# Optimization experiments

Measured on AMD Instinct MI355X. Metric: run time of the kernel, lower is better.

The kernel has to match this reference:

```python
import jax, jax.numpy as jnp
import numpy as np

B, S, D, H, O = 64, 512, 1024, 1024, 1024

def setup_inputs() -> dict:
    key = jax.random.key(0)
    k1, k2, k3 = jax.random.split(key, 3)
    x = jax.random.normal(k1, (B, S, D), dtype=jnp.float32)
    Wg = jax.random.normal(k2, (D + H, 3 * H), dtype=jnp.float32) / np.sqrt(D + H)
    bg = jnp.zeros((3 * H,), dtype=jnp.float32)
    Wc = jax.random.normal(k3, (H, O), dtype=jnp.float32) / np.sqrt(H)
    bc = jnp.zeros((O,), dtype=jnp.float32)
    return {"x": x, "Wg": Wg, "bg": bg, "Wc": Wc, "bc": bc}

def reference(x, Wg, bg, Wc, bc):
    # GRU cell matching the torch module: network = Linear(D+H, 3H)
    def step(h, x_t):
        combined = jnp.concatenate([x_t, h], axis=1)            # [B, D+H]
        gates = combined @ Wg + bg                              # [B, 3H]
        r_g, z_g, n_g = jnp.split(gates, 3, axis=1)
        r = jax.nn.sigmoid(r_g)
        z = jax.nn.sigmoid(z_g)
        n = jnp.tanh(n_g + r * h)
        h_next = (1 - z) * n + z * h
        return h_next, h_next

    h0 = jnp.zeros((x.shape[0], Wc.shape[0]), dtype=x.dtype)
    xs = jnp.swapaxes(x, 0, 1)                                  # [S, B, D]
    _, hs = jax.lax.scan(step, h0, xs)                          # hs: [S, B, H]
    outputs = jnp.swapaxes(hs, 0, 1)                            # [B, S, H]
    return outputs @ Wc + bc                                    # [B, S, O]
```

## Files before the change

kernel.cpp:

```cpp
#include <hip/hip_runtime.h>
#include <hip/hip_bf16.h>
#include <stdint.h>

#define BB   64
#define SS   512
#define DD   1024
#define HH   1024
#define TH3  3072
#define TCH  32

using frag8 = __attribute__((ext_vector_type(8))) short;
using f32x4 = __attribute__((ext_vector_type(4))) float;

__device__ __forceinline__ void split_bf16(float v, short& hi, short& lo) {
    uint32_t u = __float_as_uint(v);
    uint32_t uh = u & 0xFFFF0000u;
    float fl = v - __uint_as_float(uh);
    hi = (short)(uh >> 16);
    lo = (short)(__float_as_uint(fl) >> 16);
}

__device__ __forceinline__ float bf2f(unsigned short u) {
    union { uint32_t i; float f; } v;
    v.i = ((uint32_t)u) << 16;
    return v.f;
}

__global__ __launch_bounds__(256) void prep_w(
    const float* __restrict__ Wg, short* __restrict__ Wt_hi,
    short* __restrict__ Wt_lo)
{
    int idx = blockIdx.x * 256 + threadIdx.x;
    int lane = idx & 63;
    int f = idx >> 6;
    int kt = f & 63;
    int fg = f >> 6;
    int g = fg % 3;
    int jb = fg / 3;
    int krow = kt * 32 + (lane >> 4) * 8;
    int col = g * HH + jb * 16 + (lane & 15);
    size_t dst = (size_t)f * 512 + (size_t)lane * 8;
#pragma unroll
    for (int j = 0; j < 8; ++j) {
        float v = Wg[(size_t)(krow + j) * TH3 + col];
        short hi, lo;
        split_bf16(v, hi, lo);
        Wt_hi[dst + j] = hi;
        Wt_lo[dst + j] = lo;
    }
}

__global__ __launch_bounds__(256) void gx_gemm(
    const short* __restrict__ Wt_hi, const short* __restrict__ Wt_lo,
    const float* __restrict__ x,
    const float* __restrict__ bg,
    float* __restrict__ gx,
    int t0)
{
    const int tid = threadIdx.x;
    const int lane = tid & 63;
    const int w = tid >> 6;
    const int jb = blockIdx.x & 63;
    const int tl = blockIdx.x >> 6;
    const int t = t0 + tl;
    const int m0 = w * 16;
    const int mrow = m0 + (lane & 15);
    const int kq = (lane >> 4) * 8;

    f32x4 accr = {0.f, 0.f, 0.f, 0.f};
    f32x4 accz = {0.f, 0.f, 0.f, 0.f};
    f32x4 accn = {0.f, 0.f, 0.f, 0.f};
    const size_t fbase = (size_t)jb * 3 * 64;
    const float* xrow = x + ((size_t)mrow * SS + t) * DD;

    for (int kt = 0; kt < 32; ++kt) {
        const float* xp = xrow + kt * 32 + kq;
        float xv[8];
        *(float4*)&xv[0] = *(const float4*)xp;
        *(float4*)&xv[4] = *(const float4*)(xp + 4);
        frag8 a_hi, a_lo;
#pragma unroll
        for (int j = 0; j < 8; ++j) {
            short hi, lo;
            split_bf16(xv[j], hi, lo);
            a_hi[j] = hi;
            a_lo[j] = lo;
        }
#pragma unroll
        for (int g = 0; g < 3; ++g) {
            size_t base = (fbase + (size_t)g * 64 + kt) * 512 + (size_t)lane * 8;
            frag8 b_hi = *(const frag8*)(Wt_hi + base);
            frag8 b_lo = *(const frag8*)(Wt_lo + base);
            f32x4 acc = (g == 0) ? accr : (g == 1) ? accz : accn;
            acc = __builtin_amdgcn_mfma_f32_16x16x32_bf16(a_hi, b_hi, acc, 0, 0, 0);
            acc = __builtin_amdgcn_mfma_f32_16x16x32_bf16(a_hi, b_lo, acc, 0, 0, 0);
            acc = __builtin_amdgcn_mfma_f32_16x16x32_bf16(a_lo, b_hi, acc, 0, 0, 0);
            if (g == 0) accr = acc; else if (g == 1) accz = acc; else accn = acc;
        }
    }

    const int col = jb * 16 + (lane & 15);
    const int rbase = m0 + (lane >> 4) * 4;
    const float b_r = bg[col];
    const float b_z = bg[HH + col];
    const float b_n = bg[2 * HH + col];
#pragma unroll
    for (int reg = 0; reg < 4; ++reg) {
        int m = rbase + reg;
        float* gp = gx + ((size_t)tl * BB + m) * TH3;
        gp[col] = accr[reg] + b_r;
        gp[HH + col] = accz[reg] + b_z;
        gp[2 * HH + col] = accn[reg] + b_n;
    }
}

__global__ __launch_bounds__(256) void gru_step_h(
    const short* __restrict__ Wt_hi, const short* __restrict__ Wt_lo,
    const float* __restrict__ gx,
    const float* __restrict__ h_f,
    const short* __restrict__ h_hi,
    const short* __restrict__ h_lo,
    float* __restrict__ hn_f,
    short* __restrict__ hn_hi, short* __restrict__ hn_lo,
    __hip_bfloat16* __restrict__ hs,
    int t, int tl)
{
    __shared__ float red[12][256];

    const int tid = threadIdx.x;
    const int lane = tid & 63;
    const int w = tid >> 6;
    const int jb = blockIdx.x & 63;
    const int mt = blockIdx.x >> 6;
    const int m0 = mt * 16;
    const int mrow = m0 + (lane & 15);
    const int kq = (lane >> 4) * 8;

    const int lv = tid >> 2;
    const int reg = tid & 3;
    const int ecol = jb * 16 + (lv & 15);
    const int em = m0 + ((lv >> 4) << 2) + reg;
    const float* gp = gx + ((size_t)tl * BB + em) * TH3 + ecol;
    const float gxr = gp[0];
    const float gxz = gp[HH];
    const float gxn = gp[2 * HH];
    const float hold = h_f[(size_t)em * HH + ecol];

    f32x4 accr = {0.f, 0.f, 0.f, 0.f};
    f32x4 accz = {0.f, 0.f, 0.f, 0.f};
    f32x4 accn = {0.f, 0.f, 0.f, 0.f};
    const size_t fbase = (size_t)jb * 3 * 64;
    const short* hrh = h_hi + (size_t)mrow * HH;
    const short* hrl = h_lo + (size_t)mrow * HH;

#pragma unroll
    for (int i = 0; i < 8; ++i) {
        const int kt = w * 8 + i;
        frag8 a_hi = *(const frag8*)(hrh + kt * 32 + kq);
        frag8 a_lo = *(const frag8*)(hrl + kt * 32 + kq);
#pragma unroll
        for (int g = 0; g < 3; ++g) {
            size_t base = (fbase + (size_t)g * 64 + 32 + kt) * 512 + (size_t)lane * 8;
            frag8 b_hi = *(const frag8*)(Wt_hi + base);
            frag8 b_lo = *(const frag8*)(Wt_lo + base);
            f32x4 acc = (g == 0) ? accr : (g == 1) ? accz : accn;
            acc = __builtin_amdgcn_mfma_f32_16x16x32_bf16(a_hi, b_hi, acc, 0, 0, 0);
            acc = __builtin_amdgcn_mfma_f32_16x16x32_bf16(a_hi, b_lo, acc, 0, 0, 0);
            acc = __builtin_amdgcn_mfma_f32_16x16x32_bf16(a_lo, b_hi, acc, 0, 0, 0);
            if (g == 0) accr = acc; else if (g == 1) accz = acc; else accn = acc;
        }
    }

    *(f32x4*)&red[w * 3 + 0][lane * 4] = accr;
    *(f32x4*)&red[w * 3 + 1][lane * 4] = accz;
    *(f32x4*)&red[w * 3 + 2][lane * 4] = accn;
    __syncthreads();

    float rg = gxr + red[0][tid] + red[3][tid] + red[6][tid] + red[9][tid];
    float zg = gxz + red[1][tid] + red[4][tid] + red[7][tid] + red[10][tid];
    float ng = gxn + red[2][tid] + red[5][tid] + red[8][tid] + red[11][tid];

    float r = 1.f / (1.f + __expf(-rg));
    float z = 1.f / (1.f + __expf(-zg));
    float na = ng + r * hold;
    float n = 1.f - 2.f / (1.f + __expf(2.f * na));
    float hn = (1.f - z) * n + z * hold;

    hn_f[(size_t)em * HH + ecol] = hn;
    short hi, lo;
    split_bf16(hn, hi, lo);
    hn_hi[(size_t)em * HH + ecol] = hi;
    hn_lo[(size_t)em * HH + ecol] = lo;
    hs[((size_t)em * SS + t) * HH + ecol] = __float2bfloat16(hn);
}

#define BM 128
#define BN 128
#define BK 8

__global__ __launch_bounds__(256) void out_gemm(
    const __hip_bfloat16* __restrict__ A, const float* __restrict__ Bm,
    const float* __restrict__ bias, float* __restrict__ C)
{
    __shared__ float As[BK][BM + 4];
    __shared__ float Bs[BK][BN + 4];

    const int tid = threadIdx.x;
    const int bx = blockIdx.x;
    const int by = blockIdx.y;

    const int arow = tid >> 1;
    const int acol = (tid & 1) * 4;
    const int brow = tid >> 5;
    const int bcol = (tid & 31) * 4;

    const int tx8 = (tid & 15) * 8;
    const int ty8 = (tid >> 4) * 8;

    float acc[8][8];
#pragma unroll
    for (int i = 0; i < 8; ++i)
#pragma unroll
        for (int j = 0; j < 8; ++j) acc[i][j] = 0.f;

    const unsigned short* Aptr =
        (const unsigned short*)A + (size_t)(by * BM + arow) * HH + acol;
    const float* Bptr = Bm + (size_t)brow * HH + bx * BN + bcol;

    for (int k0 = 0; k0 < HH; k0 += BK) {
        ushort4 au = *(const ushort4*)Aptr;
        float4 bv = *(const float4*)Bptr;
        As[acol + 0][arow] = bf2f(au.x);
        As[acol + 1][arow] = bf2f(au.y);
        As[acol + 2][arow] = bf2f(au.z);
        As[acol + 3][arow] = bf2f(au.w);
        *(float4*)&Bs[brow][bcol] = bv;
        __syncthreads();

#pragma unroll
        for (int k = 0; k < BK; ++k) {
            float a[8], bvv[8];
            *(float4*)&a[0] = *(const float4*)&As[k][ty8];
            *(float4*)&a[4] = *(const float4*)&As[k][ty8 + 4];
            *(float4*)&bvv[0] = *(const float4*)&Bs[k][tx8];
            *(float4*)&bvv[4] = *(const float4*)&Bs[k][tx8 + 4];
#pragma unroll
            for (int i = 0; i < 8; ++i)
#pragma unroll
                for (int j = 0; j < 8; ++j)
                    acc[i][j] += a[i] * bvv[j];
        }
        __syncthreads();
        Aptr += BK;
        Bptr += (size_t)BK * HH;
    }

    float bv8[8];
#pragma unroll
    for (int j = 0; j < 8; ++j) bv8[j] = bias[bx * BN + tx8 + j];

#pragma unroll
    for (int i = 0; i < 8; ++i) {
        float* cptr = C + (size_t)(by * BM + ty8 + i) * HH + bx * BN + tx8;
        float4 v0, v1;
        v0.x = acc[i][0] + bv8[0];
        v0.y = acc[i][1] + bv8[1];
        v0.z = acc[i][2] + bv8[2];
        v0.w = acc[i][3] + bv8[3];
        v1.x = acc[i][4] + bv8[4];
        v1.y = acc[i][5] + bv8[5];
        v1.z = acc[i][6] + bv8[6];
        v1.w = acc[i][7] + bv8[7];
        *(float4*)cptr = v0;
        *(float4*)(cptr + 4) = v1;
    }
}

extern "C" void kernel_launch(void* const* d_in, const int* in_sizes, int n_in,
                              void* d_out, int out_size, void* d_ws, size_t ws_size,
                              hipStream_t stream) {
    const float* x  = (const float*)d_in[0];
    const float* Wg = (const float*)d_in[1];
    const float* bg = (const float*)d_in[2];
    const float* Wc = (const float*)d_in[3];
    const float* bc = (const float*)d_in[4];
    float* out = (float*)d_out;

    char* ws = (char*)d_ws;
    __hip_bfloat16* hs = (__hip_bfloat16*)ws;
    short* Wt_hi = (short*)(ws + 67108864);
    short* Wt_lo = (short*)(ws + 67108864 + 12582912);
    char* state = ws + 67108864 + 2 * 12582912;
    const size_t SET = 524288;
    float* gx = (float*)(state + 2 * SET);

    float* hf[2];  short* hhi[2]; short* hlo[2];
    for (int p = 0; p < 2; ++p) {
        hf[p]  = (float*)(state + p * SET);
        hhi[p] = (short*)(state + p * SET + 262144);
        hlo[p] = (short*)(state + p * SET + 393216);
    }

    hipMemsetAsync(state, 0, SET, stream);

    prep_w<<<3072, 256, 0, stream>>>(Wg, Wt_hi, Wt_lo);

    for (int t0 = 0; t0 < SS; t0 += TCH) {
        gx_gemm<<<TCH * 64, 256, 0, stream>>>(Wt_hi, Wt_lo, x, bg, gx, t0);
        for (int tl = 0; tl < TCH; ++tl) {
            int t = t0 + tl;
            int c = t & 1, n = c ^ 1;
            gru_step_h<<<256, 256, 0, stream>>>(
                Wt_hi, Wt_lo, gx,
                hf[c], hhi[c], hlo[c],
                hf[n], hhi[n], hlo[n],
                hs, t, tl);
        }
    }

    {
        dim3 g2(HH / BN, (BB * SS) / BM);
        out_gemm<<<g2, 256, 0, stream>>>(hs, Wc, bc, out);
    }
}
```

Measured before the change: 6.752 ms.

## Move output projection to bf16 MFMA and register-tile the input-gate GEMM

The scalar FP32 shared-memory output GEMM is replaced by an MFMA kernel. It uses bf16 hs and a hi/lo split of Wc (two MFMAs per tile), with Wc pre-swizzled into fragment layout by a new prep kernel that reuses the gx workspace. The gx_gemm kernel is also register-tiled so that each wave computes 2x2 16x16 tiles, which reuses A and B fragments and launches fewer blocks. Dropping the lo term for hs keeps the earlier bf16 rounding of hs while taking the output GEMM off the vector ALUs, but it adds another split-precision approximation for Wc.

```diff
diff --git a/kernel.cpp b/kernel.cpp
--- a/kernel.cpp
+++ b/kernel.cpp
@@ -18,12 +18,6 @@
     float fl = v - __uint_as_float(uh);
     hi = (short)(uh >> 16);
     lo = (short)(__float_as_uint(fl) >> 16);
-}
-
-__device__ __forceinline__ float bf2f(unsigned short u) {
-    union { uint32_t i; float f; } v;
-    v.i = ((uint32_t)u) << 16;
-    return v.f;
 }
 
 __global__ __launch_bounds__(256) void prep_w(
@@ -50,6 +44,28 @@
     }
 }
 
+__global__ __launch_bounds__(256) void prep_wc(
+    const float* __restrict__ Wc, short* __restrict__ Wct_hi,
+    short* __restrict__ Wct_lo)
+{
+    int idx = blockIdx.x * 256 + threadIdx.x;
+    int lane = idx & 63;
+    int f = idx >> 6;
+    int kt = f & 31;
+    int jb = f >> 5;
+    int krow = kt * 32 + (lane >> 4) * 8;
+    int col = jb * 16 + (lane & 15);
+    size_t dst = (size_t)f * 512 + (size_t)lane * 8;
+#pragma unroll
+    for (int j = 0; j < 8; ++j) {
+        float v = Wc[(size_t)(krow + j) * HH + col];
+        short hi, lo;
+        split_bf16(v, hi, lo);
+        Wct_hi[dst + j] = hi;
+        Wct_lo[dst + j] = lo;
+    }
+}
+
 __global__ __launch_bounds__(256) void gx_gemm(
     const short* __restrict__ Wt_hi, const short* __restrict__ Wt_lo,
     const float* __restrict__ x,
@@ -60,57 +76,79 @@
     const int tid = threadIdx.x;
     const int lane = tid & 63;
     const int w = tid >> 6;
-    const int jb = blockIdx.x & 63;
-    const int tl = blockIdx.x >> 6;
+    const int jbg = blockIdx.x & 15;
+    const int tl = blockIdx.x >> 4;
     const int t = t0 + tl;
-    const int m0 = w * 16;
-    const int mrow = m0 + (lane & 15);
+    const int m0 = (w & 1) * 32;
+    const int jbb = jbg * 4 + (w >> 1) * 2;
     const int kq = (lane >> 4) * 8;
 
-    f32x4 accr = {0.f, 0.f, 0.f, 0.f};
-    f32x4 accz = {0.f, 0.f, 0.f, 0.f};
-    f32x4 accn = {0.f, 0.f, 0.f, 0.f};
-    const size_t fbase = (size_t)jb * 3 * 64;
-    const float* xrow = x + ((size_t)mrow * SS + t) * DD;
+    f32x4 acc[2][2][3];
+#pragma unroll
+    for (int mi = 0; mi < 2; ++mi)
+#pragma unroll
+        for (int jp = 0; jp < 2; ++jp)
+#pragma unroll
+            for (int g = 0; g < 3; ++g)
+                acc[mi][jp][g] = (f32x4){0.f, 0.f, 0.f, 0.f};
+
+    const float* xr0 = x + ((size_t)(m0 + (lane & 15)) * SS + t) * DD;
+    const float* xr1 = xr0 + (size_t)16 * SS * DD;
 
     for (int kt = 0; kt < 32; ++kt) {
-        const float* xp = xrow + kt * 32 + kq;
-        float xv[8];
-        *(float4*)&xv[0] = *(const float4*)xp;
-        *(float4*)&xv[4] = *(const float4*)(xp + 4);
-        frag8 a_hi, a_lo;
-#pragma unroll
-        for (int j = 0; j < 8; ++j) {
-            short hi, lo;
-            split_bf16(xv[j], hi, lo);
-            a_hi[j] = hi;
-            a_lo[j] = lo;
-        }
+        frag8 ah[2], al[2];
+#pragma unroll
+        for (int mi = 0; mi < 2; ++mi) {
+            const float* xp = (mi == 0 ? xr0 : xr1) + kt * 32 + kq;
+            float xv[8];
+            *(float4*)&xv[0] = *(const float4*)xp;
+            *(float4*)&xv[4] = *(const float4*)(xp + 4);
+#pragma unroll
+            for (int j = 0; j < 8; ++j) {
+                short hi, lo;
+                split_bf16(xv[j], hi, lo);
+                ah[mi][j] = hi;
+                al[mi][j] = lo;
+            }
+        }
+#pragma unroll
+        for (int jp = 0; jp < 2; ++jp) {
+#pragma unroll
+            for (int g = 0; g < 3; ++g) {
+                size_t base =
+                    (((size_t)(jbb + jp) * 3 + g) * 64 + kt) * 512 + (size_t)lane * 8;
+                frag8 bh = *(const frag8*)(Wt_hi + base);
+                frag8 bl = *(const frag8*)(Wt_lo + base);
+#pragma unroll
+                for (int mi = 0; mi < 2; ++mi) {
+                    f32x4 a = acc[mi][jp][g];
+                    a = __builtin_amdgcn_mfma_f32_16x16x32_bf16(ah[mi], bh, a, 0, 0, 0);
+                    a = __builtin_amdgcn_mfma_f32_16x16x32_bf16(ah[mi], bl, a, 0, 0, 0);
+                    a = __builtin_amdgcn_mfma_f32_16x16x32_bf16(al[mi], bh, a, 0, 0, 0);
+                    acc[mi][jp][g] = a;
+                }
+            }
+        }
+    }
+
+    const int lcol = lane & 15;
+    const int rq = (lane >> 4) * 4;
+#pragma unroll
+    for (int jp = 0; jp < 2; ++jp) {
+        const int col = (jbb + jp) * 16 + lcol;
 #pragma unroll
         for (int g = 0; g < 3; ++g) {
-            size_t base = (fbase + (size_t)g * 64 + kt) * 512 + (size_t)lane * 8;
-            frag8 b_hi = *(const frag8*)(Wt_hi + base);
-            frag8 b_lo = *(const frag8*)(Wt_lo + base);
-            f32x4 acc = (g == 0) ? accr : (g == 1) ? accz : accn;
-            acc = __builtin_amdgcn_mfma_f32_16x16x32_bf16(a_hi, b_hi, acc, 0, 0, 0);
-            acc = __builtin_amdgcn_mfma_f32_16x16x32_bf16(a_hi, b_lo, acc, 0, 0, 0);
-            acc = __builtin_amdgcn_mfma_f32_16x16x32_bf16(a_lo, b_hi, acc, 0, 0, 0);
-            if (g == 0) accr = acc; else if (g == 1) accz = acc; else accn = acc;
-        }
-    }
-
-    const int col = jb * 16 + (lane & 15);
-    const int rbase = m0 + (lane >> 4) * 4;
-    const float b_r = bg[col];
-    const float b_z = bg[HH + col];
-    const float b_n = bg[2 * HH + col];
-#pragma unroll
-    for (int reg = 0; reg < 4; ++reg) {
-        int m = rbase + reg;
-        float* gp = gx + ((size_t)tl * BB + m) * TH3;
-        gp[col] = accr[reg] + b_r;
-        gp[HH + col] = accz[reg] + b_z;
-        gp[2 * HH + col] = accn[reg] + b_n;
+            const float bias = bg[g * HH + col];
+#pragma unroll
+            for (int mi = 0; mi < 2; ++mi) {
+#pragma unroll
+                for (int reg = 0; reg < 4; ++reg) {
+                    int m = m0 + mi * 16 + rq + reg;
+                    gx[((size_t)tl * BB + m) * TH3 + g * HH + col] =
+                        acc[mi][jp][g][reg] + bias;
+                }
+            }
+        }
     }
 }
 
@@ -194,85 +232,64 @@
     hs[((size_t)em * SS + t) * HH + ecol] = __float2bfloat16(hn);
 }
 
-#define BM 128
-#define BN 128
-#define BK 8
-
-__global__ __launch_bounds__(256) void out_gemm(
-    const __hip_bfloat16* __restrict__ A, const float* __restrict__ Bm,
-    const float* __restrict__ bias, float* __restrict__ C)
-{
-    __shared__ float As[BK][BM + 4];
-    __shared__ float Bs[BK][BN + 4];
-
+__global__ __launch_bounds__(256) void out_mfma(
+    const short* __restrict__ Wct_hi, const short* __restrict__ Wct_lo,
+    const __hip_bfloat16* __restrict__ hs,
+    const float* __restrict__ bc, float* __restrict__ out)
+{
     const int tid = threadIdx.x;
-    const int bx = blockIdx.x;
-    const int by = blockIdx.y;
-
-    const int arow = tid >> 1;
-    const int acol = (tid & 1) * 4;
-    const int brow = tid >> 5;
-    const int bcol = (tid & 31) * 4;
-
-    const int tx8 = (tid & 15) * 8;
-    const int ty8 = (tid >> 4) * 8;
-
-    float acc[8][8];
-#pragma unroll
-    for (int i = 0; i < 8; ++i)
-#pragma unroll
-        for (int j = 0; j < 8; ++j) acc[i][j] = 0.f;
-
-    const unsigned short* Aptr =
-        (const unsigned short*)A + (size_t)(by * BM + arow) * HH + acol;
-    const float* Bptr = Bm + (size_t)brow * HH + bx * BN + bcol;
-
-    for (int k0 = 0; k0 < HH; k0 += BK) {
-        ushort4 au = *(const ushort4*)Aptr;
-        float4 bv = *(const float4*)Bptr;
-        As[acol + 0][arow] = bf2f(au.x);
-        As[acol + 1][arow] = bf2f(au.y);
-        As[acol + 2][arow] = bf2f(au.z);
-        As[acol + 3][arow] = bf2f(au.w);
-        *(float4*)&Bs[brow][bcol] = bv;
-        __syncthreads();
-
-#pragma unroll
-        for (int k = 0; k < BK; ++k) {
-            float a[8], bvv[8];
-            *(float4*)&a[0] = *(const float4*)&As[k][ty8];
-            *(float4*)&a[4] = *(const float4*)&As[k][ty8 + 4];
-            *(float4*)&bvv[0] = *(const float4*)&Bs[k][tx8];
-            *(float4*)&bvv[4] = *(const float4*)&Bs[k][tx8 + 4];
-#pragma unroll
-            for (int i = 0; i < 8; ++i)
-#pragma unroll
-                for (int j = 0; j < 8; ++j)
-                    acc[i][j] += a[i] * bvv[j];
-        }
-        __syncthreads();
-        Aptr += BK;
-        Bptr += (size_t)BK * HH;
-    }
-
-    float bv8[8];
-#pragma unroll
-    for (int j = 0; j < 8; ++j) bv8[j] = bias[bx * BN + tx8 + j];
-
-#pragma unroll
-    for (int i = 0; i < 8; ++i) {
-        float* cptr = C + (size_t)(by * BM + ty8 + i) * HH + bx * BN + tx8;
-        float4 v0, v1;
-        v0.x = acc[i][0] + bv8[0];
-        v0.y = acc[i][1] + bv8[1];
-        v0.z = acc[i][2] + bv8[2];
-        v0.w = acc[i][3] + bv8[3];
-        v1.x = acc[i][4] + bv8[4];
-        v1.y = acc[i][5] + bv8[5];
-        v1.z = acc[i][6] + bv8[6];
-        v1.w = acc[i][7] + bv8[7];
-        *(float4*)cptr = v0;
-        *(float4*)(cptr + 4) = v1;
+    const int lane = tid & 63;
+    const int w = tid >> 6;
+    const int nb = blockIdx.x & 7;
+    const int mb = blockIdx.x >> 3;
+    const int r0 = mb * 128 + (w & 1) * 64;
+    const int jb0 = nb * 8 + (w >> 1) * 4;
+    const int kq = (lane >> 4) * 8;
+
+    f32x4 acc[4][4];
+#pragma unroll
+    for (int i = 0; i < 4; ++i)
+#pragma unroll
+        for (int j = 0; j < 4; ++j) acc[i][j] = (f32x4){0.f, 0.f, 0.f, 0.f};
+
+    const short* ar[4];
+#pragma unroll
+    for (int i = 0; i < 4; ++i)
+        ar[i] = (const short*)hs +
+                (size_t)(r0 + i * 16 + (lane & 15)) * HH + kq;
+
+    for (int kt = 0; kt < 32; ++kt) {
+        frag8 a[4];
+#pragma unroll
+        for (int i = 0; i < 4; ++i)
+            a[i] = *(const frag8*)(ar[i] + kt * 32);
+#pragma unroll
+        for (int j = 0; j < 4; ++j) {
+            size_t base = ((size_t)(jb0 + j) * 32 + kt) * 512 + (size_t)lane * 8;
+            frag8 bh = *(const frag8*)(Wct_hi + base);
+            frag8 bl = *(const frag8*)(Wct_lo + base);
+#pragma unroll
+            for (int i = 0; i < 4; ++i) {
+                acc[i][j] = __builtin_amdgcn_mfma_f32_16x16x32_bf16(a[i], bh, acc[i][j], 0, 0, 0);
+                acc[i][j] = __builtin_amdgcn_mfma_f32_16x16x32_bf16(a[i], bl, acc[i][j], 0, 0, 0);
+            }
+        }
+    }
+
+    const int lcol = lane & 15;
+    const int rq = (lane >> 4) * 4;
+#pragma unroll
+    for (int j = 0; j < 4; ++j) {
+        const int col = (jb0 + j) * 16 + lcol;
+        const float bias = bc[col];
+#pragma unroll
+        for (int i = 0; i < 4; ++i) {
+#pragma unroll
+            for (int reg = 0; reg < 4; ++reg) {
+                int row = r0 + i * 16 + rq + reg;
+                out[(size_t)row * HH + col] = acc[i][j][reg] + bias;
+            }
+        }
     }
 }
 
@@ -293,6 +310,8 @@
     char* state = ws + 67108864 + 2 * 12582912;
     const size_t SET = 524288;
     float* gx = (float*)(state + 2 * SET);
+    short* Wct_hi = (short*)gx;
+    short* Wct_lo = Wct_hi + 1048576;
 
     float* hf[2];  short* hhi[2]; short* hlo[2];
     for (int p = 0; p < 2; ++p) {
@@ -306,7 +325,7 @@
     prep_w<<<3072, 256, 0, stream>>>(Wg, Wt_hi, Wt_lo);
 
     for (int t0 = 0; t0 < SS; t0 += TCH) {
-        gx_gemm<<<TCH * 64, 256, 0, stream>>>(Wt_hi, Wt_lo, x, bg, gx, t0);
+        gx_gemm<<<512, 256, 0, stream>>>(Wt_hi, Wt_lo, x, bg, gx, t0);
         for (int tl = 0; tl < TCH; ++tl) {
             int t = t0 + tl;
             int c = t & 1, n = c ^ 1;
@@ -319,7 +338,7 @@
     }
 
     {
-        dim3 g2(HH / BN, (BB * SS) / BM);
-        out_gemm<<<g2, 256, 0, stream>>>(hs, Wc, bc, out);
-    }
-}
+        prep_wc<<<512, 256, 0, stream>>>(Wc, Wct_hi, Wct_lo);
+        out_mfma<<<2048, 256, 0, stream>>>(Wct_hi, Wct_lo, hs, bc, out);
+    }
+}
```

New measurement: 5.518 ms. 18.3% less time.
